# Kernel optimization log

Measured on AMD Instinct MI355X. Metric: run time of the kernel, lower is better.

## Reference

```python
import jax, jax.numpy as jnp
import numpy as np

B, H, W, C = 8, 256, 256, 96
WS, SS, NH = 8, 4, 6          # window_size, shift_size, num_heads
CH = C // NH                   # head dim = 16
NP_ = WS * WS                  # patches per window = 64
NW = (H // WS) * (W // WS)     # windows per image = 1024
SCALE = CH ** -0.5
EPS = 1e-5
NEG = -1e9


def _relative_position_index():
    coords = np.stack(np.meshgrid(np.arange(WS), np.arange(WS), indexing='ij')).reshape(2, -1)
    rel = (coords[:, :, None] - coords[:, None, :]).transpose(1, 2, 0).astype(np.int64)  # (np,np,2)
    rel[..., 0] += WS - 1
    rel[..., 0] *= 2 * WS - 1
    rel[..., 1] += WS - 1
    return rel.sum(-1)  # (NP_, NP_)


def _attn_mask():
    m = np.zeros((H, W), dtype=np.float32)
    if SS != 0:
        sl = (slice(0, -WS), slice(-WS, -SS), slice(-SS, None))
        cnt = 0
        for hs in sl:
            for ws_ in sl:
                m[hs, ws_] = cnt
                cnt += 1
    mw = m.reshape(H // WS, WS, W // WS, WS).transpose(0, 2, 1, 3).reshape(NW, NP_)
    am = mw[:, None, :] - mw[:, :, None]           # (NW, NP_, NP_)
    np.einsum('nii->ni', am)[...] = 1.0            # blind-spot diagonal
    return np.where(am != 0, NEG, 0.0).astype(np.float32)


REL_IDX = _relative_position_index()
MASK = jnp.asarray(_attn_mask())


def _layer_norm(x, g, b):
    mu = jnp.mean(x, axis=-1, keepdims=True)
    var = jnp.mean(jnp.square(x - mu), axis=-1, keepdims=True)
    return (x - mu) * jax.lax.rsqrt(var + EPS) * g + b


def setup_inputs() -> dict:
    rng = jax.random.key(0)
    ks = jax.random.split(rng, 12)
    d = dict(
        query=jax.random.normal(ks[0], (B, H, W, C), jnp.float32),
        key=jax.random.normal(ks[1], (B, H, W, C), jnp.float32),
        value=jax.random.normal(ks[2], (B, H, W, C), jnp.float32),
        rpb_table=jax.random.normal(ks[3], ((2 * WS - 1) ** 2, NH), jnp.float32) * 0.02,
        norm_g=jnp.ones((C,), jnp.float32),
        norm_b=jnp.zeros((C,), jnp.float32),
        projW=jax.random.normal(ks[4], (C, C), jnp.float32) * 0.02,
        projb=jnp.zeros((C,), jnp.float32),
        norm2_g=jnp.ones((C,), jnp.float32),
        norm2_b=jnp.zeros((C,), jnp.float32),
        fc1W=jax.random.normal(ks[5], (C, C), jnp.float32) * 0.02,
        fc1b=jnp.zeros((C,), jnp.float32),
        fc2W=jax.random.normal(ks[6], (C, C), jnp.float32) * 0.02,
        fc2b=jnp.zeros((C,), jnp.float32),
    )
    return d


def _window_partition(x):
    # (B,H,W,C) -> (B*NW, NP_, C)
    x = x.reshape(B, H // WS, WS, W // WS, WS, C).transpose(0, 1, 3, 2, 4, 5)
    return x.reshape(B * NW, NP_, C)


def reference(query, key, value, rpb_table, norm_g, norm_b, projW, projb,
              norm2_g, norm2_b, fc1W, fc1b, fc2W, fc2b):
    shift = lambda t: jnp.roll(t, (-SS, -SS), axis=(1, 2))
    q, k, v = (_window_partition(shift(t)) for t in (query, key, value))

    # head split: (B*NW, NH, NP_, CH)
    heads = lambda t: t.reshape(B * NW, NP_, NH, CH).transpose(0, 2, 1, 3)
    q, k, v = heads(q) * SCALE, heads(k), heads(v)

    attn = jnp.einsum('wnik,wnjk->wnij', q, k)                       # (B*NW, NH, NP_, NP_)
    bias = rpb_table[REL_IDX].transpose(2, 0, 1)                     # (NH, NP_, NP_)
    attn = attn + bias[None]
    attn = attn.reshape(B, NW, NH, NP_, NP_) + MASK[None, :, None]
    attn = jax.nn.softmax(attn.reshape(B * NW, NH, NP_, NP_), axis=-1)

    out = jnp.einsum('wnij,wnjk->wnik', attn, v) + q                 # residual with scaled q
    # 'nw nh (ws1 ws2) ch -> nw ws1 ws2 (nh ch)'
    out = out.reshape(B * NW, NH, WS, WS, CH).transpose(0, 2, 3, 1, 4).reshape(B * NW, WS, WS, C)
    out = _layer_norm(out, norm_g, norm_b)
    out = out @ projW.T + projb

    # window reverse: (B*NW, WS, WS, C) -> (B,H,W,C), then unshift
    out = out.reshape(B, H // WS, W // WS, WS, WS, C).transpose(0, 1, 3, 2, 4, 5).reshape(B, H, W, C)
    out = jnp.roll(out, (SS, SS), axis=(1, 2))

    # out + Mlp(norm2(out)); Mlp = Linear -> GELU -> Linear
    h = _layer_norm(out, norm2_g, norm2_b)
    h = jax.nn.gelu(h @ fc1W.T + fc1b, approximate=False)
    h = h @ fc2W.T + fc2b
    return out + h
```

## Files before the change

### kernel.cpp

```cpp
#include <hip/hip_runtime.h>
#include <math.h>

#define WSZ 8
#define SSZ 4
#define NHD 6
#define CHD 16
#define CCH 96
#define NPT 64
#define HH  256
#define WWI 256
#define QSCALE 0.25f
#define NEGV (-1e9f)
#define EPSV 1e-5f

__global__ __launch_bounds__(384, 3)
void attn_kernel(const float* __restrict__ q_g, const float* __restrict__ k_g,
                 const float* __restrict__ v_g, const float* __restrict__ rpb,
                 const float* __restrict__ ng,  const float* __restrict__ nb,
                 const float* __restrict__ pw,  const float* __restrict__ pb,
                 float* __restrict__ out)
{
    __shared__ __align__(16) float sK[NHD * NPT * CHD];
    __shared__ __align__(16) float sV[NHD * NPT * CHD];
    __shared__ float sX[NPT * 101];
    __shared__ float sMu[NPT], sRs[NPT];
    __shared__ int   sRid[NPT];

    const int n  = blockIdx.x;
    const int b  = n >> 10;
    const int nw = n & 1023;
    const int wh = nw >> 5, ww = nw & 31;
    const int t  = threadIdx.x;
    const int head = __builtin_amdgcn_readfirstlane(t >> 6);
    const int p  = t & 63;

    const long long img_base = (long long)b * (HH * WWI * CCH);

    #pragma unroll
    for (int i = 0; i < 4; ++i) {
        int idx4 = t + i * 384;
        int pp   = idx4 / 24;
        int cc   = (idx4 % 24) * 4;
        int r = pp >> 3, c2 = pp & 7;
        int gh = (wh * 8 + r  + SSZ) & 255;
        int gw = (ww * 8 + c2 + SSZ) & 255;
        long long ga = img_base + (long long)(gh * WWI + gw) * CCH + cc;
        float4 kv = *(const float4*)(k_g + ga);
        float4 vv = *(const float4*)(v_g + ga);
        int hd = cc >> 4, ch = cc & 15;
        *(float4*)(&sK[hd * (NPT * CHD) + pp * CHD + ch]) = kv;
        *(float4*)(&sV[hd * (NPT * CHD) + pp * CHD + ch]) = vv;
    }
    if (t < 64) {
        int r = t >> 3, c2 = t & 7;
        int hh2 = wh * 8 + r;
        int ww2 = ww * 8 + c2;
        int rh = (hh2 < HH - WSZ) ? 0 : ((hh2 < HH - SSZ) ? 1 : 2);
        int rw = (ww2 < WWI - WSZ) ? 0 : ((ww2 < WWI - SSZ) ? 1 : 2);
        sRid[t] = rh * 3 + rw;
    }

    const int r1 = p >> 3, c1 = p & 7;
    float4 qr0, qr1, qr2, qr3;
    {
        int gh = (wh * 8 + r1 + SSZ) & 255;
        int gw = (ww * 8 + c1 + SSZ) & 255;
        long long ga = img_base + (long long)(gh * WWI + gw) * CCH + head * CHD;
        qr0 = *(const float4*)(q_g + ga);
        qr1 = *(const float4*)(q_g + ga + 4);
        qr2 = *(const float4*)(q_g + ga + 8);
        qr3 = *(const float4*)(q_g + ga + 12);
        qr0.x *= QSCALE; qr0.y *= QSCALE; qr0.z *= QSCALE; qr0.w *= QSCALE;
        qr1.x *= QSCALE; qr1.y *= QSCALE; qr1.z *= QSCALE; qr1.w *= QSCALE;
        qr2.x *= QSCALE; qr2.y *= QSCALE; qr2.z *= QSCALE; qr2.w *= QSCALE;
        qr3.x *= QSCALE; qr3.y *= QSCALE; qr3.z *= QSCALE; qr3.w *= QSCALE;
    }
    __syncthreads();

    float s[64];
    const int rid_i = sRid[p];
    const float* biasbase = rpb + ((r1 + 7) * 15 + (c1 + 7)) * NHD + head;
    const float* kh = &sK[head * (NPT * CHD)];
    #pragma unroll
    for (int j = 0; j < 64; ++j) {
        const float4 k0 = *(const float4*)(kh + j * 16);
        const float4 k1 = *(const float4*)(kh + j * 16 + 4);
        const float4 k2 = *(const float4*)(kh + j * 16 + 8);
        const float4 k3 = *(const float4*)(kh + j * 16 + 12);
        float d0 = qr0.x * k0.x + qr0.y * k0.y + qr0.z * k0.z + qr0.w * k0.w;
        float d1 = qr1.x * k1.x + qr1.y * k1.y + qr1.z * k1.z + qr1.w * k1.w;
        float d2 = qr2.x * k2.x + qr2.y * k2.y + qr2.z * k2.z + qr2.w * k2.w;
        float d3 = qr3.x * k3.x + qr3.y * k3.y + qr3.z * k3.z + qr3.w * k3.w;
        int r2 = j >> 3, c2 = j & 7;
        float bias = biasbase[-(r2 * 15 + c2) * NHD];
        float msk = (sRid[j] != rid_i || j == p) ? NEGV : 0.0f;
        s[j] = (d0 + d1) + (d2 + d3) + bias + msk;
    }

    float m8[8];
    #pragma unroll
    for (int j = 0; j < 8; ++j) m8[j] = s[j];
    #pragma unroll
    for (int j = 8; j < 64; ++j) m8[j & 7] = fmaxf(m8[j & 7], s[j]);
    float mx = fmaxf(fmaxf(fmaxf(m8[0], m8[1]), fmaxf(m8[2], m8[3])),
                     fmaxf(fmaxf(m8[4], m8[5]), fmaxf(m8[6], m8[7])));
    float l8[8];
    #pragma unroll
    for (int j = 0; j < 8; ++j) { s[j] = __expf(s[j] - mx); l8[j] = s[j]; }
    #pragma unroll
    for (int j = 8; j < 64; ++j) { s[j] = __expf(s[j] - mx); l8[j & 7] += s[j]; }
    float l = ((l8[0] + l8[1]) + (l8[2] + l8[3])) + ((l8[4] + l8[5]) + (l8[6] + l8[7]));
    float invl = 1.0f / l;

    float4 a0 = {0,0,0,0}, a1 = {0,0,0,0}, a2 = {0,0,0,0}, a3 = {0,0,0,0};
    const float* vh = &sV[head * (NPT * CHD)];
    #pragma unroll
    for (int j = 0; j < 64; ++j) {
        float pj = s[j];
        const float4 v0 = *(const float4*)(vh + j * 16);
        const float4 v1 = *(const float4*)(vh + j * 16 + 4);
        const float4 v2 = *(const float4*)(vh + j * 16 + 8);
        const float4 v3 = *(const float4*)(vh + j * 16 + 12);
        a0.x += pj * v0.x; a0.y += pj * v0.y; a0.z += pj * v0.z; a0.w += pj * v0.w;
        a1.x += pj * v1.x; a1.y += pj * v1.y; a1.z += pj * v1.z; a1.w += pj * v1.w;
        a2.x += pj * v2.x; a2.y += pj * v2.y; a2.z += pj * v2.z; a2.w += pj * v2.w;
        a3.x += pj * v3.x; a3.y += pj * v3.y; a3.z += pj * v3.z; a3.w += pj * v3.w;
    }
    {
        float* xr = &sX[p * 101 + head * CHD];
        xr[0]  = a0.x * invl + qr0.x; xr[1]  = a0.y * invl + qr0.y;
        xr[2]  = a0.z * invl + qr0.z; xr[3]  = a0.w * invl + qr0.w;
        xr[4]  = a1.x * invl + qr1.x; xr[5]  = a1.y * invl + qr1.y;
        xr[6]  = a1.z * invl + qr1.z; xr[7]  = a1.w * invl + qr1.w;
        xr[8]  = a2.x * invl + qr2.x; xr[9]  = a2.y * invl + qr2.y;
        xr[10] = a2.z * invl + qr2.z; xr[11] = a2.w * invl + qr2.w;
        xr[12] = a3.x * invl + qr3.x; xr[13] = a3.y * invl + qr3.y;
        xr[14] = a3.z * invl + qr3.z; xr[15] = a3.w * invl + qr3.w;
    }
    __syncthreads();

    if (t < 64) {
        float sum = 0.f, sq = 0.f;
        for (int c = 0; c < 96; ++c) {
            float x = sX[t * 101 + c];
            sum += x; sq += x * x;
        }
        float mu  = sum * (1.0f / 96.0f);
        float var = sq * (1.0f / 96.0f) - mu * mu;
        sMu[t] = mu;
        sRs[t] = 1.0f / sqrtf(var + EPSV);
    }
    __syncthreads();

    {
        float mu = sMu[p], rs = sRs[p];
        #pragma unroll
        for (int i = 0; i < 16; ++i) {
            int c = head * CHD + i;
            float x = sX[p * 101 + c];
            sX[p * 101 + c] = (x - mu) * rs * ng[c] + nb[c];
        }
    }
    __syncthreads();

    {
        float acc[16];
        #pragma unroll
        for (int i = 0; i < 16; ++i) acc[i] = 0.f;
        const float* xrow  = &sX[p * 101];
        const float* wbase = pw + head * 16 * 96;
        #pragma unroll 4
        for (int c = 0; c < 96; ++c) {
            float xv = xrow[c];
            #pragma unroll
            for (int i = 0; i < 16; ++i) acc[i] += xv * wbase[i * 96 + c];
        }
        int gh = (wh * 8 + r1 + SSZ) & 255;
        int gw = (ww * 8 + c1 + SSZ) & 255;
        float* op = out + img_base + (long long)(gh * WWI + gw) * CCH + head * 16;
        #pragma unroll
        for (int i = 0; i < 16; i += 4) {
            float4 v;
            v.x = acc[i + 0] + pb[head * 16 + i + 0];
            v.y = acc[i + 1] + pb[head * 16 + i + 1];
            v.z = acc[i + 2] + pb[head * 16 + i + 2];
            v.w = acc[i + 3] + pb[head * 16 + i + 3];
            *(float4*)(op + i) = v;
        }
    }
}

__global__ __launch_bounds__(256, 3)
void mlp_kernel(float* __restrict__ io,
                const float* __restrict__ g2, const float* __restrict__ b2,
                const float* __restrict__ w1, const float* __restrict__ bb1,
                const float* __restrict__ w2, const float* __restrict__ bb2)
{
    __shared__ float sX[64 * 101];
    __shared__ float sH[64 * 97];
    __shared__ float sMu[64], sRs[64];

    const int t = threadIdx.x;
    const long long base = (long long)blockIdx.x * (64 * 96);

    #pragma unroll
    for (int i = 0; i < 6; ++i) {
        int idx4 = t + i * 256;
        int pp = idx4 / 24, cc = (idx4 % 24) * 4;
        float4 x = *(const float4*)(io + base + (long long)idx4 * 4);
        float* d = &sX[pp * 101 + cc];
        d[0] = x.x; d[1] = x.y; d[2] = x.z; d[3] = x.w;
    }
    __syncthreads();

    if (t < 64) {
        float sum = 0.f, sq = 0.f;
        for (int c = 0; c < 96; ++c) {
            float x = sX[t * 101 + c];
            sum += x; sq += x * x;
        }
        float mu  = sum * (1.0f / 96.0f);
        float var = sq * (1.0f / 96.0f) - mu * mu;
        sMu[t] = mu;
        sRs[t] = 1.0f / sqrtf(var + EPSV);
    }
    __syncthreads();

    const int grp = __builtin_amdgcn_readfirstlane(t >> 6);
    const int p   = t & 63;
    const float mu = sMu[p], rs = sRs[p];

    {
        float acc[24];
        #pragma unroll
        for (int i = 0; i < 24; ++i) acc[i] = 0.f;
        const float* xrow = &sX[p * 101];
        const float* w1b  = w1 + grp * 24 * 96;
        #pragma unroll 4
        for (int c = 0; c < 96; ++c) {
            float xv = (xrow[c] - mu) * rs * g2[c] + b2[c];
            #pragma unroll
            for (int i = 0; i < 24; ++i) acc[i] += xv * w1b[i * 96 + c];
        }
        #pragma unroll
        for (int i = 0; i < 24; ++i) {
            float h = acc[i] + bb1[grp * 24 + i];
            h = 0.5f * h * (1.0f + erff(h * 0.70710678118654752f));
            sH[p * 97 + grp * 24 + i] = h;
        }
    }
    __syncthreads();

    {
        float acc[24];
        #pragma unroll
        for (int i = 0; i < 24; ++i) acc[i] = 0.f;
        const float* hrow = &sH[p * 97];
        const float* w2b  = w2 + grp * 24 * 96;
        #pragma unroll 4
        for (int o = 0; o < 96; ++o) {
            float hv = hrow[o];
            #pragma unroll
            for (int i = 0; i < 24; ++i) acc[i] += hv * w2b[i * 96 + o];
        }
        #pragma unroll
        for (int i = 0; i < 24; i += 4) {
            int o = grp * 24 + i;
            float4 v;
            v.x = sX[p * 101 + o + 0] + acc[i + 0] + bb2[o + 0];
            v.y = sX[p * 101 + o + 1] + acc[i + 1] + bb2[o + 1];
            v.z = sX[p * 101 + o + 2] + acc[i + 2] + bb2[o + 2];
            v.w = sX[p * 101 + o + 3] + acc[i + 3] + bb2[o + 3];
            *(float4*)(io + base + p * 96 + o) = v;
        }
    }
}

extern "C" void kernel_launch(void* const* d_in, const int* in_sizes, int n_in,
                              void* d_out, int out_size, void* d_ws, size_t ws_size,
                              hipStream_t stream) {
    (void)in_sizes; (void)n_in; (void)out_size; (void)d_ws; (void)ws_size;
    const float* q_g  = (const float*)d_in[0];
    const float* k_g  = (const float*)d_in[1];
    const float* v_g  = (const float*)d_in[2];
    const float* rpb  = (const float*)d_in[3];
    const float* ng   = (const float*)d_in[4];
    const float* nb   = (const float*)d_in[5];
    const float* pw   = (const float*)d_in[6];
    const float* pb   = (const float*)d_in[7];
    const float* g2   = (const float*)d_in[8];
    const float* b2   = (const float*)d_in[9];
    const float* w1   = (const float*)d_in[10];
    const float* bb1  = (const float*)d_in[11];
    const float* w2   = (const float*)d_in[12];
    const float* bb2  = (const float*)d_in[13];
    float* out = (float*)d_out;

    attn_kernel<<<dim3(8192), dim3(384), 0, stream>>>(q_g, k_g, v_g, rpb, ng, nb, pw, pb, out);
    mlp_kernel<<<dim3(8192), dim3(256), 0, stream>>>(out, g2, b2, w1, bb1, w2, bb2);
}
```

Measured before the change: 1.763 ms.

## Fuse attention and MLP into one per-window kernel with online softmax

Merges the attention+projection kernel and the MLP kernel into a single kernel, so the intermediate (B,H,W,C) tensor never makes a round trip through global memory. This works because the roll-back is pointwise and the MLP is per-pixel, so each window can be finished in place. The softmax becomes an online, chunked version to cut register pressure, allowing launch bounds of 4 blocks per CU. LayerNorm statistics now come from per-head partial sums reduced in shared memory, and K/V/X/H share one shared buffer. In exchange, the MLP runs with 384 threads per window and the block does more sequential work.

```diff
diff --git a/kernel.cpp b/kernel.cpp
--- a/kernel.cpp
+++ b/kernel.cpp
@@ -12,17 +12,21 @@
 #define QSCALE 0.25f
 #define NEGV (-1e9f)
 #define EPSV 1e-5f
-
-__global__ __launch_bounds__(384, 3)
-void attn_kernel(const float* __restrict__ q_g, const float* __restrict__ k_g,
-                 const float* __restrict__ v_g, const float* __restrict__ rpb,
-                 const float* __restrict__ ng,  const float* __restrict__ nb,
-                 const float* __restrict__ pw,  const float* __restrict__ pb,
-                 float* __restrict__ out)
+#define XP 97
+
+__global__ __launch_bounds__(384, 4)
+void fused_block_kernel(const float* __restrict__ q_g, const float* __restrict__ k_g,
+                        const float* __restrict__ v_g, const float* __restrict__ rpb,
+                        const float* __restrict__ ng,  const float* __restrict__ nb,
+                        const float* __restrict__ pw,  const float* __restrict__ pb,
+                        const float* __restrict__ g2,  const float* __restrict__ b2,
+                        const float* __restrict__ w1,  const float* __restrict__ bb1,
+                        const float* __restrict__ w2,  const float* __restrict__ bb2,
+                        float* __restrict__ out)
 {
-    __shared__ __align__(16) float sK[NHD * NPT * CHD];
-    __shared__ __align__(16) float sV[NHD * NPT * CHD];
-    __shared__ float sX[NPT * 101];
+    __shared__ __align__(16) float sB[2 * NPT * XP];
+    __shared__ float sPS[NHD * NPT];
+    __shared__ float sPQ[NHD * NPT];
     __shared__ float sMu[NPT], sRs[NPT];
     __shared__ int   sRid[NPT];
 
@@ -36,24 +40,24 @@
 
     const long long img_base = (long long)b * (HH * WWI * CCH);
 
+    float* sK = sB;
+    float* sV = sB + NPT * CCH;
+
     #pragma unroll
     for (int i = 0; i < 4; ++i) {
         int idx4 = t + i * 384;
         int pp   = idx4 / 24;
         int cc   = (idx4 % 24) * 4;
-        int r = pp >> 3, c2 = pp & 7;
-        int gh = (wh * 8 + r  + SSZ) & 255;
+        int rr = pp >> 3, c2 = pp & 7;
+        int gh = (wh * 8 + rr + SSZ) & 255;
         int gw = (ww * 8 + c2 + SSZ) & 255;
         long long ga = img_base + (long long)(gh * WWI + gw) * CCH + cc;
-        float4 kv = *(const float4*)(k_g + ga);
-        float4 vv = *(const float4*)(v_g + ga);
-        int hd = cc >> 4, ch = cc & 15;
-        *(float4*)(&sK[hd * (NPT * CHD) + pp * CHD + ch]) = kv;
-        *(float4*)(&sV[hd * (NPT * CHD) + pp * CHD + ch]) = vv;
+        *(float4*)(&sK[idx4 * 4]) = *(const float4*)(k_g + ga);
+        *(float4*)(&sV[idx4 * 4]) = *(const float4*)(v_g + ga);
     }
     if (t < 64) {
-        int r = t >> 3, c2 = t & 7;
-        int hh2 = wh * 8 + r;
+        int rr = t >> 3, c2 = t & 7;
+        int hh2 = wh * 8 + rr;
         int ww2 = ww * 8 + c2;
         int rh = (hh2 < HH - WSZ) ? 0 : ((hh2 < HH - SSZ) ? 1 : 2);
         int rw = (ww2 < WWI - WSZ) ? 0 : ((ww2 < WWI - SSZ) ? 1 : 2);
@@ -61,217 +65,195 @@
     }
 
     const int r1 = p >> 3, c1 = p & 7;
-    float4 qr0, qr1, qr2, qr3;
-    {
-        int gh = (wh * 8 + r1 + SSZ) & 255;
-        int gw = (ww * 8 + c1 + SSZ) & 255;
-        long long ga = img_base + (long long)(gh * WWI + gw) * CCH + head * CHD;
-        qr0 = *(const float4*)(q_g + ga);
-        qr1 = *(const float4*)(q_g + ga + 4);
-        qr2 = *(const float4*)(q_g + ga + 8);
-        qr3 = *(const float4*)(q_g + ga + 12);
-        qr0.x *= QSCALE; qr0.y *= QSCALE; qr0.z *= QSCALE; qr0.w *= QSCALE;
-        qr1.x *= QSCALE; qr1.y *= QSCALE; qr1.z *= QSCALE; qr1.w *= QSCALE;
-        qr2.x *= QSCALE; qr2.y *= QSCALE; qr2.z *= QSCALE; qr2.w *= QSCALE;
-        qr3.x *= QSCALE; qr3.y *= QSCALE; qr3.z *= QSCALE; qr3.w *= QSCALE;
-    }
-    __syncthreads();
-
-    float s[64];
+    const int gh1 = (wh * 8 + r1 + SSZ) & 255;
+    const int gw1 = (ww * 8 + c1 + SSZ) & 255;
+    float q[16];
+    {
+        long long ga = img_base + (long long)(gh1 * WWI + gw1) * CCH + head * CHD;
+        #pragma unroll
+        for (int i = 0; i < 16; i += 4) {
+            float4 v4 = *(const float4*)(q_g + ga + i);
+            q[i+0] = v4.x * QSCALE; q[i+1] = v4.y * QSCALE;
+            q[i+2] = v4.z * QSCALE; q[i+3] = v4.w * QSCALE;
+        }
+    }
+    __syncthreads();
+
     const int rid_i = sRid[p];
     const float* biasbase = rpb + ((r1 + 7) * 15 + (c1 + 7)) * NHD + head;
-    const float* kh = &sK[head * (NPT * CHD)];
-    #pragma unroll
-    for (int j = 0; j < 64; ++j) {
-        const float4 k0 = *(const float4*)(kh + j * 16);
-        const float4 k1 = *(const float4*)(kh + j * 16 + 4);
-        const float4 k2 = *(const float4*)(kh + j * 16 + 8);
-        const float4 k3 = *(const float4*)(kh + j * 16 + 12);
-        float d0 = qr0.x * k0.x + qr0.y * k0.y + qr0.z * k0.z + qr0.w * k0.w;
-        float d1 = qr1.x * k1.x + qr1.y * k1.y + qr1.z * k1.z + qr1.w * k1.w;
-        float d2 = qr2.x * k2.x + qr2.y * k2.y + qr2.z * k2.z + qr2.w * k2.w;
-        float d3 = qr3.x * k3.x + qr3.y * k3.y + qr3.z * k3.z + qr3.w * k3.w;
-        int r2 = j >> 3, c2 = j & 7;
-        float bias = biasbase[-(r2 * 15 + c2) * NHD];
-        float msk = (sRid[j] != rid_i || j == p) ? NEGV : 0.0f;
-        s[j] = (d0 + d1) + (d2 + d3) + bias + msk;
-    }
-
-    float m8[8];
-    #pragma unroll
-    for (int j = 0; j < 8; ++j) m8[j] = s[j];
-    #pragma unroll
-    for (int j = 8; j < 64; ++j) m8[j & 7] = fmaxf(m8[j & 7], s[j]);
-    float mx = fmaxf(fmaxf(fmaxf(m8[0], m8[1]), fmaxf(m8[2], m8[3])),
-                     fmaxf(fmaxf(m8[4], m8[5]), fmaxf(m8[6], m8[7])));
-    float l8[8];
-    #pragma unroll
-    for (int j = 0; j < 8; ++j) { s[j] = __expf(s[j] - mx); l8[j] = s[j]; }
-    #pragma unroll
-    for (int j = 8; j < 64; ++j) { s[j] = __expf(s[j] - mx); l8[j & 7] += s[j]; }
-    float l = ((l8[0] + l8[1]) + (l8[2] + l8[3])) + ((l8[4] + l8[5]) + (l8[6] + l8[7]));
-    float invl = 1.0f / l;
-
-    float4 a0 = {0,0,0,0}, a1 = {0,0,0,0}, a2 = {0,0,0,0}, a3 = {0,0,0,0};
-    const float* vh = &sV[head * (NPT * CHD)];
-    #pragma unroll
-    for (int j = 0; j < 64; ++j) {
-        float pj = s[j];
-        const float4 v0 = *(const float4*)(vh + j * 16);
-        const float4 v1 = *(const float4*)(vh + j * 16 + 4);
-        const float4 v2 = *(const float4*)(vh + j * 16 + 8);
-        const float4 v3 = *(const float4*)(vh + j * 16 + 12);
-        a0.x += pj * v0.x; a0.y += pj * v0.y; a0.z += pj * v0.z; a0.w += pj * v0.w;
-        a1.x += pj * v1.x; a1.y += pj * v1.y; a1.z += pj * v1.z; a1.w += pj * v1.w;
-        a2.x += pj * v2.x; a2.y += pj * v2.y; a2.z += pj * v2.z; a2.w += pj * v2.w;
-        a3.x += pj * v3.x; a3.y += pj * v3.y; a3.z += pj * v3.z; a3.w += pj * v3.w;
-    }
-    {
-        float* xr = &sX[p * 101 + head * CHD];
-        xr[0]  = a0.x * invl + qr0.x; xr[1]  = a0.y * invl + qr0.y;
-        xr[2]  = a0.z * invl + qr0.z; xr[3]  = a0.w * invl + qr0.w;
-        xr[4]  = a1.x * invl + qr1.x; xr[5]  = a1.y * invl + qr1.y;
-        xr[6]  = a1.z * invl + qr1.z; xr[7]  = a1.w * invl + qr1.w;
-        xr[8]  = a2.x * invl + qr2.x; xr[9]  = a2.y * invl + qr2.y;
-        xr[10] = a2.z * invl + qr2.z; xr[11] = a2.w * invl + qr2.w;
-        xr[12] = a3.x * invl + qr3.x; xr[13] = a3.y * invl + qr3.y;
-        xr[14] = a3.z * invl + qr3.z; xr[15] = a3.w * invl + qr3.w;
-    }
-    __syncthreads();
-
+
+    float acc[16];
+    #pragma unroll
+    for (int i = 0; i < 16; ++i) acc[i] = 0.f;
+    float mrun = -1e30f, lrun = 0.f;
+
+    for (int j0 = 0; j0 < 64; j0 += 16) {
+        float sc[16];
+        #pragma unroll
+        for (int jj = 0; jj < 16; ++jj) {
+            const int j = j0 + jj;
+            const float* kr = &sK[j * CCH + head * CHD];
+            float4 k0 = *(const float4*)(kr +  0);
+            float4 k1 = *(const float4*)(kr +  4);
+            float4 k2 = *(const float4*)(kr +  8);
+            float4 k3 = *(const float4*)(kr + 12);
+            float d0 = q[0]*k0.x + q[1]*k0.y + q[2]*k0.z + q[3]*k0.w;
+            float d1 = q[4]*k1.x + q[5]*k1.y + q[6]*k1.z + q[7]*k1.w;
+            float d2 = q[8]*k2.x + q[9]*k2.y + q[10]*k2.z + q[11]*k2.w;
+            float d3 = q[12]*k3.x + q[13]*k3.y + q[14]*k3.z + q[15]*k3.w;
+            const int r2 = j >> 3, cc2 = j & 7;
+            float bias = biasbase[-(r2 * 15 + cc2) * NHD];
+            float msk = (sRid[j] != rid_i || j == p) ? NEGV : 0.0f;
+            sc[jj] = (d0 + d1) + (d2 + d3) + bias + msk;
+        }
+        float m01 = fmaxf(sc[0],  sc[1]),  m23 = fmaxf(sc[2],  sc[3]);
+        float m45 = fmaxf(sc[4],  sc[5]),  m67 = fmaxf(sc[6],  sc[7]);
+        float m89 = fmaxf(sc[8],  sc[9]),  mab = fmaxf(sc[10], sc[11]);
+        float mcd = fmaxf(sc[12], sc[13]), mef = fmaxf(sc[14], sc[15]);
+        float mq = fmaxf(fmaxf(fmaxf(m01, m23), fmaxf(m45, m67)),
+                         fmaxf(fmaxf(m89, mab), fmaxf(mcd, mef)));
+        float mnew  = fmaxf(mrun, mq);
+        float scale = __expf(mrun - mnew);
+        lrun *= scale;
+        #pragma unroll
+        for (int i = 0; i < 16; ++i) acc[i] *= scale;
+        #pragma unroll
+        for (int jj = 0; jj < 16; ++jj) {
+            const int j = j0 + jj;
+            float pj = __expf(sc[jj] - mnew);
+            lrun += pj;
+            const float* vr = &sV[j * CCH + head * CHD];
+            float4 v0 = *(const float4*)(vr +  0);
+            float4 v1 = *(const float4*)(vr +  4);
+            float4 v2 = *(const float4*)(vr +  8);
+            float4 v3 = *(const float4*)(vr + 12);
+            acc[0] += pj*v0.x;  acc[1] += pj*v0.y;  acc[2] += pj*v0.z;  acc[3] += pj*v0.w;
+            acc[4] += pj*v1.x;  acc[5] += pj*v1.y;  acc[6] += pj*v1.z;  acc[7] += pj*v1.w;
+            acc[8] += pj*v2.x;  acc[9] += pj*v2.y;  acc[10]+= pj*v2.z;  acc[11]+= pj*v2.w;
+            acc[12]+= pj*v3.x;  acc[13]+= pj*v3.y;  acc[14]+= pj*v3.z;  acc[15]+= pj*v3.w;
+        }
+        mrun = mnew;
+    }
+    {
+        float invl = 1.0f / lrun;
+        #pragma unroll
+        for (int i = 0; i < 16; ++i) acc[i] = acc[i] * invl + q[i];
+    }
+    {
+        float s1 = 0.f, s2 = 0.f;
+        #pragma unroll
+        for (int i = 0; i < 16; ++i) { s1 += acc[i]; s2 += acc[i] * acc[i]; }
+        sPS[head * 64 + p] = s1;
+        sPQ[head * 64 + p] = s2;
+    }
+    __syncthreads();
     if (t < 64) {
-        float sum = 0.f, sq = 0.f;
-        for (int c = 0; c < 96; ++c) {
-            float x = sX[t * 101 + c];
-            sum += x; sq += x * x;
-        }
-        float mu  = sum * (1.0f / 96.0f);
+        float su = 0.f, sq = 0.f;
+        #pragma unroll
+        for (int h = 0; h < NHD; ++h) { su += sPS[h * 64 + t]; sq += sPQ[h * 64 + t]; }
+        float mu  = su * (1.0f / 96.0f);
         float var = sq * (1.0f / 96.0f) - mu * mu;
         sMu[t] = mu;
         sRs[t] = 1.0f / sqrtf(var + EPSV);
     }
     __syncthreads();
-
     {
         float mu = sMu[p], rs = sRs[p];
         #pragma unroll
         for (int i = 0; i < 16; ++i) {
-            int c = head * CHD + i;
-            float x = sX[p * 101 + c];
-            sX[p * 101 + c] = (x - mu) * rs * ng[c] + nb[c];
-        }
-    }
-    __syncthreads();
-
-    {
-        float acc[16];
-        #pragma unroll
-        for (int i = 0; i < 16; ++i) acc[i] = 0.f;
-        const float* xrow  = &sX[p * 101];
-        const float* wbase = pw + head * 16 * 96;
+            int ch = head * CHD + i;
+            sB[p * XP + ch] = (acc[i] - mu) * rs * ng[ch] + nb[ch];
+        }
+    }
+    __syncthreads();
+
+    float P[16];
+    #pragma unroll
+    for (int i = 0; i < 16; ++i) P[i] = pb[head * CHD + i];
+    {
+        const float* xrow = &sB[p * XP];
+        const float* wb   = pw + head * CHD * CCH;
         #pragma unroll 4
-        for (int c = 0; c < 96; ++c) {
+        for (int c = 0; c < CCH; ++c) {
             float xv = xrow[c];
             #pragma unroll
-            for (int i = 0; i < 16; ++i) acc[i] += xv * wbase[i * 96 + c];
-        }
-        int gh = (wh * 8 + r1 + SSZ) & 255;
-        int gw = (ww * 8 + c1 + SSZ) & 255;
-        float* op = out + img_base + (long long)(gh * WWI + gw) * CCH + head * 16;
-        #pragma unroll
-        for (int i = 0; i < 16; i += 4) {
-            float4 v;
-            v.x = acc[i + 0] + pb[head * 16 + i + 0];
-            v.y = acc[i + 1] + pb[head * 16 + i + 1];
-            v.z = acc[i + 2] + pb[head * 16 + i + 2];
-            v.w = acc[i + 3] + pb[head * 16 + i + 3];
-            *(float4*)(op + i) = v;
-        }
-    }
-}
-
-__global__ __launch_bounds__(256, 3)
-void mlp_kernel(float* __restrict__ io,
-                const float* __restrict__ g2, const float* __restrict__ b2,
-                const float* __restrict__ w1, const float* __restrict__ bb1,
-                const float* __restrict__ w2, const float* __restrict__ bb2)
-{
-    __shared__ float sX[64 * 101];
-    __shared__ float sH[64 * 97];
-    __shared__ float sMu[64], sRs[64];
-
-    const int t = threadIdx.x;
-    const long long base = (long long)blockIdx.x * (64 * 96);
-
-    #pragma unroll
-    for (int i = 0; i < 6; ++i) {
-        int idx4 = t + i * 256;
-        int pp = idx4 / 24, cc = (idx4 % 24) * 4;
-        float4 x = *(const float4*)(io + base + (long long)idx4 * 4);
-        float* d = &sX[pp * 101 + cc];
-        d[0] = x.x; d[1] = x.y; d[2] = x.z; d[3] = x.w;
-    }
-    __syncthreads();
-
+            for (int i = 0; i < 16; ++i) P[i] += xv * wb[i * CCH + c];
+        }
+    }
+    {
+        float s1 = 0.f, s2 = 0.f;
+        #pragma unroll
+        for (int i = 0; i < 16; ++i) { s1 += P[i]; s2 += P[i] * P[i]; }
+        sPS[head * 64 + p] = s1;
+        sPQ[head * 64 + p] = s2;
+    }
+    __syncthreads();
     if (t < 64) {
-        float sum = 0.f, sq = 0.f;
-        for (int c = 0; c < 96; ++c) {
-            float x = sX[t * 101 + c];
-            sum += x; sq += x * x;
-        }
-        float mu  = sum * (1.0f / 96.0f);
+        float su = 0.f, sq = 0.f;
+        #pragma unroll
+        for (int h = 0; h < NHD; ++h) { su += sPS[h * 64 + t]; sq += sPQ[h * 64 + t]; }
+        float mu  = su * (1.0f / 96.0f);
         float var = sq * (1.0f / 96.0f) - mu * mu;
         sMu[t] = mu;
         sRs[t] = 1.0f / sqrtf(var + EPSV);
     }
     __syncthreads();
-
-    const int grp = __builtin_amdgcn_readfirstlane(t >> 6);
-    const int p   = t & 63;
-    const float mu = sMu[p], rs = sRs[p];
-
-    {
-        float acc[24];
-        #pragma unroll
-        for (int i = 0; i < 24; ++i) acc[i] = 0.f;
-        const float* xrow = &sX[p * 101];
-        const float* w1b  = w1 + grp * 24 * 96;
+    {
+        float mu = sMu[p], rs = sRs[p];
+        #pragma unroll
+        for (int i = 0; i < 16; ++i) {
+            int ch = head * CHD + i;
+            sB[p * XP + ch] = (P[i] - mu) * rs * g2[ch] + b2[ch];
+        }
+    }
+    __syncthreads();
+
+    float hacc[16];
+    #pragma unroll
+    for (int i = 0; i < 16; ++i) hacc[i] = bb1[head * CHD + i];
+    {
+        const float* xrow = &sB[p * XP];
+        const float* wb   = w1 + head * CHD * CCH;
         #pragma unroll 4
-        for (int c = 0; c < 96; ++c) {
-            float xv = (xrow[c] - mu) * rs * g2[c] + b2[c];
+        for (int c = 0; c < CCH; ++c) {
+            float xv = xrow[c];
             #pragma unroll
-            for (int i = 0; i < 24; ++i) acc[i] += xv * w1b[i * 96 + c];
-        }
-        #pragma unroll
-        for (int i = 0; i < 24; ++i) {
-            float h = acc[i] + bb1[grp * 24 + i];
+            for (int i = 0; i < 16; ++i) hacc[i] += xv * wb[i * CCH + c];
+        }
+    }
+    {
+        float* sH = sB + NPT * XP;
+        #pragma unroll
+        for (int i = 0; i < 16; ++i) {
+            float h = hacc[i];
             h = 0.5f * h * (1.0f + erff(h * 0.70710678118654752f));
-            sH[p * 97 + grp * 24 + i] = h;
-        }
-    }
-    __syncthreads();
-
-    {
-        float acc[24];
-        #pragma unroll
-        for (int i = 0; i < 24; ++i) acc[i] = 0.f;
-        const float* hrow = &sH[p * 97];
-        const float* w2b  = w2 + grp * 24 * 96;
+            sH[p * XP + head * CHD + i] = h;
+        }
+    }
+    __syncthreads();
+
+    #pragma unroll
+    for (int i = 0; i < 16; ++i) hacc[i] = bb2[head * CHD + i];
+    {
+        const float* hrow = &sB[NPT * XP + p * XP];
+        const float* wb   = w2 + head * CHD * CCH;
         #pragma unroll 4
-        for (int o = 0; o < 96; ++o) {
-            float hv = hrow[o];
+        for (int c = 0; c < CCH; ++c) {
+            float hv = hrow[c];
             #pragma unroll
-            for (int i = 0; i < 24; ++i) acc[i] += hv * w2b[i * 96 + o];
-        }
-        #pragma unroll
-        for (int i = 0; i < 24; i += 4) {
-            int o = grp * 24 + i;
-            float4 v;
-            v.x = sX[p * 101 + o + 0] + acc[i + 0] + bb2[o + 0];
-            v.y = sX[p * 101 + o + 1] + acc[i + 1] + bb2[o + 1];
-            v.z = sX[p * 101 + o + 2] + acc[i + 2] + bb2[o + 2];
-            v.w = sX[p * 101 + o + 3] + acc[i + 3] + bb2[o + 3];
-            *(float4*)(io + base + p * 96 + o) = v;
+            for (int i = 0; i < 16; ++i) hacc[i] += hv * wb[i * CCH + c];
+        }
+    }
+    {
+        float* op = out + img_base + (long long)(gh1 * WWI + gw1) * CCH + head * CHD;
+        #pragma unroll
+        for (int i = 0; i < 16; i += 4) {
+            float4 v4;
+            v4.x = P[i+0] + hacc[i+0];
+            v4.y = P[i+1] + hacc[i+1];
+            v4.z = P[i+2] + hacc[i+2];
+            v4.w = P[i+3] + hacc[i+3];
+            *(float4*)(op + i) = v4;
         }
     }
 }
@@ -296,6 +278,6 @@
     const float* bb2  = (const float*)d_in[13];
     float* out = (float*)d_out;
 
-    attn_kernel<<<dim3(8192), dim3(384), 0, stream>>>(q_g, k_g, v_g, rpb, ng, nb, pw, pb, out);
-    mlp_kernel<<<dim3(8192), dim3(256), 0, stream>>>(out, g2, b2, w1, bb1, w2, bb2);
+    fused_block_kernel<<<dim3(8192), dim3(384), 0, stream>>>(
+        q_g, k_g, v_g, rpb, ng, nb, pw, pb, g2, b2, w1, bb1, w2, bb2, out);
 }
```

Measured after the change: 1.493 ms. -15.3%, faster.
